# Kernel tuning notes

Measured on AMD Instinct MI355X. Metric: run time of the kernel, lower is better.

## Reference

```python
import jax, jax.numpy as jnp
import numpy as np

B, S, E, H = 1, 2048, 1024, 16
D = E // H  # head_dim = 64


def setup_inputs() -> dict:
    key = jax.random.key(0)
    ks = jax.random.split(key, 9)
    sd = 0.02
    hidden_states = jax.random.normal(ks[0], (B, S, E), dtype=jnp.float32)
    # causal mask: positions with mask==0 are filled with -inf (per masked_fill_)
    mask = jnp.tril(jnp.ones((1, 1, S, S), dtype=bool))
    Wq = jax.random.normal(ks[1], (E, E), dtype=jnp.float32) * sd
    bq = jax.random.normal(ks[2], (E,), dtype=jnp.float32) * sd
    Wk = jax.random.normal(ks[3], (D, E), dtype=jnp.float32) * sd
    bk = jax.random.normal(ks[4], (D,), dtype=jnp.float32) * sd
    Wv = jax.random.normal(ks[5], (D, E), dtype=jnp.float32) * sd
    bv = jax.random.normal(ks[6], (D,), dtype=jnp.float32) * sd
    Wo = jax.random.normal(ks[7], (E, E), dtype=jnp.float32) * sd
    bo = jax.random.normal(ks[8], (E,), dtype=jnp.float32) * sd
    return {"hidden_states": hidden_states, "mask": mask,
            "Wq": Wq, "bq": bq, "Wk": Wk, "bk": bk,
            "Wv": Wv, "bv": bv, "Wo": Wo, "bo": bo}


def reference(hidden_states, mask, Wq, bq, Wk, bk, Wv, bv, Wo, bo):
    bsz, tgt_len, embed_dim = hidden_states.shape
    # projections (torch Linear: x @ W^T + b)
    q = hidden_states @ Wq.T + bq                       # [B, S, E]
    q = q.reshape(bsz, tgt_len, H, D).transpose(0, 2, 1, 3)  # [B, H, S, D]
    k = hidden_states @ Wk.T + bk                       # [B, S, D] shared single KV head
    v = hidden_states @ Wv.T + bv                       # [B, S, D]
    scaling = jnp.sqrt(jnp.asarray(D, dtype=hidden_states.dtype))
    # QK^T with implicit broadcast of the shared K head (instead of expand)
    scores = jnp.einsum('bhqd,bkd->bhqk', q, k) / scaling   # [B, H, S, S]
    scores = jnp.where(mask, scores, -jnp.inf)
    probs = jax.nn.softmax(scores, axis=-1)             # dropout p=0 -> identity
    attn = jnp.einsum('bhqk,bkd->bhqd', probs, v)       # [B, H, S, D]
    attn = attn.transpose(0, 2, 1, 3).reshape(bsz, tgt_len, H * D)
    return attn @ Wo.T + bo                             # [B, S, E]
```

## Files before the change

kernel.cpp:

```cpp
#include <hip/hip_runtime.h>
#include <hip/hip_bf16.h>

typedef __hip_bfloat16 bf16;
typedef __attribute__((ext_vector_type(8))) short short8;
typedef __attribute__((ext_vector_type(4))) float f32x4;

__device__ __forceinline__ short8 ld8(const void* p) { return *(const short8*)p; }
__device__ __forceinline__ void st8(void* p, short8 v) { *(short8*)p = v; }

__device__ __forceinline__ void async_cp16(bf16* lds, const bf16* g) {
    __builtin_amdgcn_global_load_lds(
        (const __attribute__((address_space(1))) unsigned int*)g,
        (__attribute__((address_space(3))) unsigned int*)lds, 16, 0, 0);
}

struct bf4 { bf16 a, b, c, d; };

__global__ void cast_kernel(const float* __restrict__ s0, bf16* __restrict__ d0, int n0_,
                            const float* __restrict__ s1, bf16* __restrict__ d1, int n1_,
                            const float* __restrict__ s2, bf16* __restrict__ d2, int n2_,
                            const float* __restrict__ s3, bf16* __restrict__ d3, int n3_,
                            const float* __restrict__ s4, bf16* __restrict__ d4, int n4_) {
    const float* srcs[5] = {s0, s1, s2, s3, s4};
    bf16* dsts[5] = {d0, d1, d2, d3, d4};
    int ns[5] = {n0_, n1_, n2_, n3_, n4_};
    int stride = gridDim.x * blockDim.x;
    int t0 = blockIdx.x * blockDim.x + threadIdx.x;
#pragma unroll
    for (int a = 0; a < 5; ++a) {
        const float4* src = (const float4*)srcs[a];
        bf4* dst = (bf4*)dsts[a];
        int n4 = ns[a] >> 2;
        for (int i = t0; i < n4; i += stride) {
            float4 v = src[i];
            bf4 o = {__float2bfloat16(v.x), __float2bfloat16(v.y),
                     __float2bfloat16(v.z), __float2bfloat16(v.w)};
            dst[i] = o;
        }
    }
}

__global__ void qkv_proj_kernel(const bf16* __restrict__ A,
                                const bf16* __restrict__ Wq, const bf16* __restrict__ Wk,
                                const bf16* __restrict__ Wv,
                                const float* __restrict__ bq, const float* __restrict__ bk,
                                const float* __restrict__ bv,
                                bf16* __restrict__ qo, bf16* __restrict__ ko,
                                bf16* __restrict__ vto, int M, int K) {
    __shared__ __align__(16) bf16 As[128][64];
    __shared__ __align__(16) bf16 Bs[64][64];
    const int nt = blockIdx.x;
    const bf16* W;
    const float* bias;
    int mode, nw0;
    if (nt < 16)      { W = Wq; bias = bq; mode = 0; nw0 = nt * 64; }
    else if (nt == 16){ W = Wk; bias = bk; mode = 1; nw0 = 0; }
    else              { W = Wv; bias = bv; mode = 2; nw0 = 0; }

    const int tid = threadIdx.x;
    const int wave = tid >> 6, lane = tid & 63;
    const int l16 = lane & 15, quad = lane >> 4;
    const int m0 = blockIdx.y * 128;
    const int lr = lane >> 3, lsw = (lane & 7) ^ (lr & 7);

    f32x4 acc[2][4];
    const f32x4 z = {0.f, 0.f, 0.f, 0.f};
#pragma unroll
    for (int mi = 0; mi < 2; ++mi)
#pragma unroll
        for (int ni = 0; ni < 4; ++ni) acc[mi][ni] = z;

    for (int k0 = 0; k0 < K; k0 += 64) {
#pragma unroll
        for (int u = 0; u < 4; ++u) {
            int t = wave * 4 + u;
            async_cp16(&As[t * 8][0], A + (size_t)(m0 + t * 8 + lr) * K + k0 + lsw * 8);
        }
#pragma unroll
        for (int u = 0; u < 2; ++u) {
            int t = wave * 2 + u;
            async_cp16(&Bs[t * 8][0], W + (size_t)(nw0 + t * 8 + lr) * K + k0 + lsw * 8);
        }
        __syncthreads();

        short8 af[2][2], bfr[2][4];
#pragma unroll
        for (int mi = 0; mi < 2; ++mi)
#pragma unroll
            for (int kc = 0; kc < 2; ++kc) {
                int R = wave * 32 + mi * 16 + l16;
                int g = kc * 4 + quad;
                af[mi][kc] = ld8(&As[R][(g ^ (R & 7)) * 8]);
            }
#pragma unroll
        for (int ni = 0; ni < 4; ++ni)
#pragma unroll
            for (int kc = 0; kc < 2; ++kc) {
                int r = ni * 16 + l16;
                int g = kc * 4 + quad;
                bfr[kc][ni] = ld8(&Bs[r][(g ^ (r & 7)) * 8]);
            }
#pragma unroll
        for (int kc = 0; kc < 2; ++kc)
#pragma unroll
            for (int mi = 0; mi < 2; ++mi)
#pragma unroll
                for (int ni = 0; ni < 4; ++ni)
                    acc[mi][ni] = __builtin_amdgcn_mfma_f32_16x16x32_bf16(
                        af[mi][kc], bfr[kc][ni], acc[mi][ni], 0, 0, 0);
        __syncthreads();
    }

#pragma unroll
    for (int mi = 0; mi < 2; ++mi)
#pragma unroll
        for (int ni = 0; ni < 4; ++ni)
#pragma unroll
            for (int r = 0; r < 4; ++r) {
                int row = m0 + wave * 32 + mi * 16 + quad * 4 + r;
                int col = ni * 16 + l16;
                float v = acc[mi][ni][r] + bias[nw0 + col];
                if (mode == 0)
                    qo[(size_t)row * 1024 + nt * 64 + col] = __float2bfloat16(v * 0.125f);
                else if (mode == 1)
                    ko[(size_t)row * 64 + col] = __float2bfloat16(v);
                else
                    vto[(size_t)col * M + row] = __float2bfloat16(v);
            }
}

__global__ void gemm_bt_mfma(const bf16* __restrict__ A, const bf16* __restrict__ W,
                             const float* __restrict__ bias, float* __restrict__ C,
                             int M, int N, int K) {
    __shared__ __align__(16) bf16 As[128][64];
    __shared__ __align__(16) bf16 Bs[64][64];
    const int tid = threadIdx.x;
    const int wave = tid >> 6, lane = tid & 63;
    const int l16 = lane & 15, quad = lane >> 4;
    const int m0 = blockIdx.y * 128, n0 = blockIdx.x * 64;
    const int lr = lane >> 3, lsw = (lane & 7) ^ (lr & 7);

    f32x4 acc[2][4];
    const f32x4 z = {0.f, 0.f, 0.f, 0.f};
#pragma unroll
    for (int mi = 0; mi < 2; ++mi)
#pragma unroll
        for (int ni = 0; ni < 4; ++ni) acc[mi][ni] = z;

    for (int k0 = 0; k0 < K; k0 += 64) {
#pragma unroll
        for (int u = 0; u < 4; ++u) {
            int t = wave * 4 + u;
            async_cp16(&As[t * 8][0], A + (size_t)(m0 + t * 8 + lr) * K + k0 + lsw * 8);
        }
#pragma unroll
        for (int u = 0; u < 2; ++u) {
            int t = wave * 2 + u;
            async_cp16(&Bs[t * 8][0], W + (size_t)(n0 + t * 8 + lr) * K + k0 + lsw * 8);
        }
        __syncthreads();

        short8 af[2][2], bfr[2][4];
#pragma unroll
        for (int mi = 0; mi < 2; ++mi)
#pragma unroll
            for (int kc = 0; kc < 2; ++kc) {
                int R = wave * 32 + mi * 16 + l16;
                int g = kc * 4 + quad;
                af[mi][kc] = ld8(&As[R][(g ^ (R & 7)) * 8]);
            }
#pragma unroll
        for (int ni = 0; ni < 4; ++ni)
#pragma unroll
            for (int kc = 0; kc < 2; ++kc) {
                int r = ni * 16 + l16;
                int g = kc * 4 + quad;
                bfr[kc][ni] = ld8(&Bs[r][(g ^ (r & 7)) * 8]);
            }
#pragma unroll
        for (int kc = 0; kc < 2; ++kc)
#pragma unroll
            for (int mi = 0; mi < 2; ++mi)
#pragma unroll
                for (int ni = 0; ni < 4; ++ni)
                    acc[mi][ni] = __builtin_amdgcn_mfma_f32_16x16x32_bf16(
                        af[mi][kc], bfr[kc][ni], acc[mi][ni], 0, 0, 0);
        __syncthreads();
    }

#pragma unroll
    for (int mi = 0; mi < 2; ++mi)
#pragma unroll
        for (int ni = 0; ni < 4; ++ni)
#pragma unroll
            for (int r = 0; r < 4; ++r) {
                int row = m0 + wave * 32 + mi * 16 + quad * 4 + r;
                int col = n0 + ni * 16 + l16;
                C[(size_t)row * N + col] = acc[mi][ni][r] + bias[col];
            }
}

__global__ void flash_mfma_kernel(const bf16* __restrict__ Q, const bf16* __restrict__ Kg,
                                  const bf16* __restrict__ VT,
                                  float* __restrict__ Opart, float* __restrict__ Lpart,
                                  int S) {
    const int s = blockIdx.x;
    int i, c;
    if (s < 32)      { c = 0; i = s; }
    else if (s < 56) { c = 1; i = s - 24; }
    else if (s < 72) { c = 2; i = s - 40; }
    else             { c = 3; i = s - 48; }

    __shared__ __align__(16) bf16 Ks[2][64][64];
    __shared__ __align__(16) bf16 Vt[2][64][64];
    __shared__ bf16 Ps[4][16][68];

    const int h = blockIdx.y;
    const int q0 = i * 64;
    const int tid = threadIdx.x;
    const int wave = tid >> 6, lane = tid & 63;
    const int l16 = lane & 15, quad = lane >> 4;
    const int lr = lane >> 3, lsw = (lane & 7) ^ (lr & 7);
    const int qrow = q0 + wave * 16;

    short8 qf[2];
#pragma unroll
    for (int kc = 0; kc < 2; ++kc)
        qf[kc] = ld8(Q + (size_t)(qrow + l16) * 1024 + h * 64 + kc * 32 + quad * 8);

    short8 onesf;
    {
        short o = (l16 == 0) ? (short)0x3F80 : (short)0;
        onesf[0]=o; onesf[1]=o; onesf[2]=o; onesf[3]=o;
        onesf[4]=o; onesf[5]=o; onesf[6]=o; onesf[7]=o;
    }

    f32x4 of[4];
    const f32x4 z = {0.f, 0.f, 0.f, 0.f};
#pragma unroll
    for (int dt = 0; dt < 4; ++dt) of[dt] = z;
    f32x4 lacc = z;

    const int jt0 = c * 8;
    const int jt1 = min(c * 8 + 8, i + 1);

    {
        const int j0 = jt0 * 64;
#pragma unroll
        for (int u = 0; u < 2; ++u) {
            int t = wave * 2 + u;
            async_cp16(&Ks[0][t * 8][0], Kg + (size_t)(j0 + t * 8 + lr) * 64 + lsw * 8);
            async_cp16(&Vt[0][t * 8][0], VT + (size_t)(t * 8 + lr) * S + j0 + lsw * 8);
        }
    }

    int buf = 0;
    for (int jt = jt0; jt < jt1; ++jt, buf ^= 1) {
        __syncthreads();
        if (jt + 1 < jt1) {
            const int j0n = (jt + 1) * 64;
#pragma unroll
            for (int u = 0; u < 2; ++u) {
                int t = wave * 2 + u;
                async_cp16(&Ks[buf ^ 1][t * 8][0], Kg + (size_t)(j0n + t * 8 + lr) * 64 + lsw * 8);
                async_cp16(&Vt[buf ^ 1][t * 8][0], VT + (size_t)(t * 8 + lr) * S + j0n + lsw * 8);
            }
        }
        const int j0 = jt * 64;

        f32x4 sc[4];
#pragma unroll
        for (int nt = 0; nt < 4; ++nt) {
            int R = nt * 16 + l16;
            sc[nt] = __builtin_amdgcn_mfma_f32_16x16x32_bf16(
                qf[0], ld8(&Ks[buf][R][(quad ^ (R & 7)) * 8]), z, 0, 0, 0);
            sc[nt] = __builtin_amdgcn_mfma_f32_16x16x32_bf16(
                qf[1], ld8(&Ks[buf][R][((4 + quad) ^ (R & 7)) * 8]), sc[nt], 0, 0, 0);
        }
        bool need_mask = (j0 + 63 > qrow);
        if (need_mask) {
#pragma unroll
            for (int nt = 0; nt < 4; ++nt)
#pragma unroll
                for (int r = 0; r < 4; ++r)
                    if (j0 + nt * 16 + l16 > qrow + quad * 4 + r) sc[nt][r] = -1e30f;
        }

#pragma unroll
        for (int nt = 0; nt < 4; ++nt)
#pragma unroll
            for (int r = 0; r < 4; ++r)
                Ps[wave][quad * 4 + r][nt * 16 + l16] = __float2bfloat16(__expf(sc[nt][r]));

        short8 pf[2];
        pf[0] = ld8(&Ps[wave][l16][quad * 8]);
        pf[1] = ld8(&Ps[wave][l16][32 + quad * 8]);

        lacc = __builtin_amdgcn_mfma_f32_16x16x32_bf16(pf[0], onesf, lacc, 0, 0, 0);
        lacc = __builtin_amdgcn_mfma_f32_16x16x32_bf16(pf[1], onesf, lacc, 0, 0, 0);

#pragma unroll
        for (int dt = 0; dt < 4; ++dt) {
            int R = dt * 16 + l16;
            of[dt] = __builtin_amdgcn_mfma_f32_16x16x32_bf16(
                pf[0], ld8(&Vt[buf][R][(quad ^ (R & 7)) * 8]), of[dt], 0, 0, 0);
            of[dt] = __builtin_amdgcn_mfma_f32_16x16x32_bf16(
                pf[1], ld8(&Vt[buf][R][((4 + quad) ^ (R & 7)) * 8]), of[dt], 0, 0, 0);
        }
    }

    float* Op = Opart + ((size_t)s * 16 + h) * 4096;
#pragma unroll
    for (int dt = 0; dt < 4; ++dt)
#pragma unroll
        for (int r = 0; r < 4; ++r) {
            int row = wave * 16 + quad * 4 + r;
            Op[row * 64 + dt * 16 + l16] = of[dt][r];
        }
    if (l16 == 0) {
        float* L = Lpart + ((size_t)s * 16 + h) * 64;
#pragma unroll
        for (int r = 0; r < 4; ++r)
            L[wave * 16 + quad * 4 + r] = lacc[r];
    }
}

__global__ void flash_merge_kernel(const float* __restrict__ Opart,
                                   const float* __restrict__ Lpart,
                                   bf16* __restrict__ attn) {
    const int i = blockIdx.x, h = blockIdx.y;
    const int nch = (i >> 3) + 1;
    const int tid = threadIdx.x;
    const int row = tid >> 2, cg = (tid & 3) * 16;

    float L = 0.f;
    for (int cc = 0; cc < nch; ++cc) {
        int s = (cc == 0) ? i : (cc == 1) ? 24 + i : (cc == 2) ? 40 + i : 48 + i;
        L += Lpart[((size_t)s * 16 + h) * 64 + row];
    }
    float inv = 1.f / L;

    float o[16];
#pragma unroll
    for (int j = 0; j < 16; ++j) o[j] = 0.f;
    for (int cc = 0; cc < nch; ++cc) {
        int s = (cc == 0) ? i : (cc == 1) ? 24 + i : (cc == 2) ? 40 + i : 48 + i;
        const float* Op = Opart + ((size_t)s * 16 + h) * 4096 + row * 64 + cg;
#pragma unroll
        for (int j = 0; j < 16; ++j) o[j] += Op[j];
    }
    bf16* dst = attn + (size_t)(i * 64 + row) * 1024 + h * 64 + cg;
#pragma unroll
    for (int j = 0; j < 16; ++j) dst[j] = __float2bfloat16(o[j] * inv);
}

extern "C" void kernel_launch(void* const* d_in, const int* in_sizes, int n_in,
                              void* d_out, int out_size, void* d_ws, size_t ws_size,
                              hipStream_t stream) {
    const int S = 2048, E = 1024, D = 64;

    const float* hs = (const float*)d_in[0];
    const float* Wq = (const float*)d_in[2];
    const float* bq = (const float*)d_in[3];
    const float* Wk = (const float*)d_in[4];
    const float* bk = (const float*)d_in[5];
    const float* Wv = (const float*)d_in[6];
    const float* bv = (const float*)d_in[7];
    const float* Wo = (const float*)d_in[8];
    const float* bo = (const float*)d_in[9];
    float* out = (float*)d_out;

    bf16* ws = (bf16*)d_ws;
    bf16* hsb = ws;
    bf16* wqb = hsb + (size_t)S * E;
    bf16* wkb = wqb + (size_t)E * E;
    bf16* wvb = wkb + (size_t)D * E;
    bf16* wob = wvb + (size_t)D * E;
    bf16* q = wob + (size_t)E * E;
    bf16* kbuf = q + (size_t)S * E;
    bf16* vt = kbuf + (size_t)S * D;
    bf16* attn = vt + (size_t)S * D;
    float* Opart = (float*)(attn + (size_t)S * E);
    float* Lpart = Opart + (size_t)1280 * 4096;

    dim3 blk(256);
    cast_kernel<<<512, blk, 0, stream>>>(hs, hsb, S * E,
                                         Wq, wqb, E * E,
                                         Wk, wkb, D * E,
                                         Wv, wvb, D * E,
                                         Wo, wob, E * E);
    qkv_proj_kernel<<<dim3(18, S / 128), blk, 0, stream>>>(hsb, wqb, wkb, wvb,
                                                           bq, bk, bv,
                                                           q, kbuf, vt, S, E);
    flash_mfma_kernel<<<dim3(80, 16), blk, 0, stream>>>(q, kbuf, vt, Opart, Lpart, S);
    flash_merge_kernel<<<dim3(32, 16), blk, 0, stream>>>(Opart, Lpart, attn);
    gemm_bt_mfma<<<dim3(E / 64, S / 128), blk, 0, stream>>>(attn, wob, bo, out, S, E, E);
}
```

Before: 160.6 us.

## Retile GEMMs to 64x64 with K=128 stages, halve flash splits, store partials in bf16

```diff
diff --git a/kernel.cpp b/kernel.cpp
--- a/kernel.cpp
+++ b/kernel.cpp
@@ -6,7 +6,6 @@
 typedef __attribute__((ext_vector_type(4))) float f32x4;
 
 __device__ __forceinline__ short8 ld8(const void* p) { return *(const short8*)p; }
-__device__ __forceinline__ void st8(void* p, short8 v) { *(short8*)p = v; }
 
 __device__ __forceinline__ void async_cp16(bf16* lds, const bf16* g) {
     __builtin_amdgcn_global_load_lds(
@@ -40,6 +39,15 @@
     }
 }
 
+#define GEMM_STAGE(dst, src_base, row0, ldk)                                   \
+    _Pragma("unroll")                                                          \
+    for (int u = 0; u < 4; ++u) {                                              \
+        int t = wave * 4 + u;                                                  \
+        int row = t * 4 + (lane >> 4);                                         \
+        int gsrc = (lane & 15) ^ (row & 15);                                   \
+        async_cp16(&dst[t * 4][0], src_base + (size_t)(row0 + row) * ldk + k0 + gsrc * 8); \
+    }
+
 __global__ void qkv_proj_kernel(const bf16* __restrict__ A,
                                 const bf16* __restrict__ Wq, const bf16* __restrict__ Wk,
                                 const bf16* __restrict__ Wv,
@@ -47,8 +55,8 @@
                                 const float* __restrict__ bv,
                                 bf16* __restrict__ qo, bf16* __restrict__ ko,
                                 bf16* __restrict__ vto, int M, int K) {
-    __shared__ __align__(16) bf16 As[128][64];
-    __shared__ __align__(16) bf16 Bs[64][64];
+    __shared__ __align__(16) bf16 As[64][128];
+    __shared__ __align__(16) bf16 Bs[64][128];
     const int nt = blockIdx.x;
     const bf16* W;
     const float* bias;
@@ -60,156 +68,117 @@
     const int tid = threadIdx.x;
     const int wave = tid >> 6, lane = tid & 63;
     const int l16 = lane & 15, quad = lane >> 4;
-    const int m0 = blockIdx.y * 128;
-    const int lr = lane >> 3, lsw = (lane & 7) ^ (lr & 7);
-
-    f32x4 acc[2][4];
+    const int m0 = blockIdx.y * 64;
+
+    f32x4 acc[4];
     const f32x4 z = {0.f, 0.f, 0.f, 0.f};
 #pragma unroll
-    for (int mi = 0; mi < 2; ++mi)
-#pragma unroll
-        for (int ni = 0; ni < 4; ++ni) acc[mi][ni] = z;
-
-    for (int k0 = 0; k0 < K; k0 += 64) {
-#pragma unroll
-        for (int u = 0; u < 4; ++u) {
-            int t = wave * 4 + u;
-            async_cp16(&As[t * 8][0], A + (size_t)(m0 + t * 8 + lr) * K + k0 + lsw * 8);
-        }
-#pragma unroll
-        for (int u = 0; u < 2; ++u) {
-            int t = wave * 2 + u;
-            async_cp16(&Bs[t * 8][0], W + (size_t)(nw0 + t * 8 + lr) * K + k0 + lsw * 8);
-        }
-        __syncthreads();
-
-        short8 af[2][2], bfr[2][4];
-#pragma unroll
-        for (int mi = 0; mi < 2; ++mi)
-#pragma unroll
-            for (int kc = 0; kc < 2; ++kc) {
-                int R = wave * 32 + mi * 16 + l16;
-                int g = kc * 4 + quad;
-                af[mi][kc] = ld8(&As[R][(g ^ (R & 7)) * 8]);
-            }
-#pragma unroll
-        for (int ni = 0; ni < 4; ++ni)
-#pragma unroll
-            for (int kc = 0; kc < 2; ++kc) {
-                int r = ni * 16 + l16;
-                int g = kc * 4 + quad;
-                bfr[kc][ni] = ld8(&Bs[r][(g ^ (r & 7)) * 8]);
-            }
-#pragma unroll
-        for (int kc = 0; kc < 2; ++kc)
-#pragma unroll
-            for (int mi = 0; mi < 2; ++mi)
-#pragma unroll
-                for (int ni = 0; ni < 4; ++ni)
-                    acc[mi][ni] = __builtin_amdgcn_mfma_f32_16x16x32_bf16(
-                        af[mi][kc], bfr[kc][ni], acc[mi][ni], 0, 0, 0);
-        __syncthreads();
-    }
-
-#pragma unroll
-    for (int mi = 0; mi < 2; ++mi)
-#pragma unroll
-        for (int ni = 0; ni < 4; ++ni)
-#pragma unroll
-            for (int r = 0; r < 4; ++r) {
-                int row = m0 + wave * 32 + mi * 16 + quad * 4 + r;
-                int col = ni * 16 + l16;
-                float v = acc[mi][ni][r] + bias[nw0 + col];
-                if (mode == 0)
-                    qo[(size_t)row * 1024 + nt * 64 + col] = __float2bfloat16(v * 0.125f);
-                else if (mode == 1)
-                    ko[(size_t)row * 64 + col] = __float2bfloat16(v);
-                else
-                    vto[(size_t)col * M + row] = __float2bfloat16(v);
-            }
+    for (int ni = 0; ni < 4; ++ni) acc[ni] = z;
+
+    for (int k0 = 0; k0 < K; k0 += 128) {
+        GEMM_STAGE(As, A, m0, K)
+        GEMM_STAGE(Bs, W, nw0, K)
+        __syncthreads();
+
+        short8 af[4], bfr[4][4];
+        {
+            int R = wave * 16 + l16;
+#pragma unroll
+            for (int kc = 0; kc < 4; ++kc)
+                af[kc] = ld8(&As[R][((kc * 4 + quad) ^ (R & 15)) * 8]);
+        }
+#pragma unroll
+        for (int ni = 0; ni < 4; ++ni) {
+            int r = ni * 16 + l16;
+#pragma unroll
+            for (int kc = 0; kc < 4; ++kc)
+                bfr[kc][ni] = ld8(&Bs[r][((kc * 4 + quad) ^ (r & 15)) * 8]);
+        }
+#pragma unroll
+        for (int kc = 0; kc < 4; ++kc)
+#pragma unroll
+            for (int ni = 0; ni < 4; ++ni)
+                acc[ni] = __builtin_amdgcn_mfma_f32_16x16x32_bf16(
+                    af[kc], bfr[kc][ni], acc[ni], 0, 0, 0);
+        __syncthreads();
+    }
+
+#pragma unroll
+    for (int ni = 0; ni < 4; ++ni)
+#pragma unroll
+        for (int r = 0; r < 4; ++r) {
+            int row = m0 + wave * 16 + quad * 4 + r;
+            int col = ni * 16 + l16;
+            float v = acc[ni][r] + bias[nw0 + col];
+            if (mode == 0)
+                qo[(size_t)row * 1024 + nt * 64 + col] = __float2bfloat16(v * 0.125f);
+            else if (mode == 1)
+                ko[(size_t)row * 64 + col] = __float2bfloat16(v);
+            else
+                vto[(size_t)col * M + row] = __float2bfloat16(v);
+        }
 }
 
 __global__ void gemm_bt_mfma(const bf16* __restrict__ A, const bf16* __restrict__ W,
                              const float* __restrict__ bias, float* __restrict__ C,
                              int M, int N, int K) {
-    __shared__ __align__(16) bf16 As[128][64];
-    __shared__ __align__(16) bf16 Bs[64][64];
+    __shared__ __align__(16) bf16 As[64][128];
+    __shared__ __align__(16) bf16 Bs[64][128];
     const int tid = threadIdx.x;
     const int wave = tid >> 6, lane = tid & 63;
     const int l16 = lane & 15, quad = lane >> 4;
-    const int m0 = blockIdx.y * 128, n0 = blockIdx.x * 64;
-    const int lr = lane >> 3, lsw = (lane & 7) ^ (lr & 7);
-
-    f32x4 acc[2][4];
+    const int m0 = blockIdx.y * 64, n0 = blockIdx.x * 64;
+
+    f32x4 acc[4];
     const f32x4 z = {0.f, 0.f, 0.f, 0.f};
 #pragma unroll
-    for (int mi = 0; mi < 2; ++mi)
-#pragma unroll
-        for (int ni = 0; ni < 4; ++ni) acc[mi][ni] = z;
-
-    for (int k0 = 0; k0 < K; k0 += 64) {
-#pragma unroll
-        for (int u = 0; u < 4; ++u) {
-            int t = wave * 4 + u;
-            async_cp16(&As[t * 8][0], A + (size_t)(m0 + t * 8 + lr) * K + k0 + lsw * 8);
-        }
-#pragma unroll
-        for (int u = 0; u < 2; ++u) {
-            int t = wave * 2 + u;
-            async_cp16(&Bs[t * 8][0], W + (size_t)(n0 + t * 8 + lr) * K + k0 + lsw * 8);
-        }
-        __syncthreads();
-
-        short8 af[2][2], bfr[2][4];
-#pragma unroll
-        for (int mi = 0; mi < 2; ++mi)
-#pragma unroll
-            for (int kc = 0; kc < 2; ++kc) {
-                int R = wave * 32 + mi * 16 + l16;
-                int g = kc * 4 + quad;
-                af[mi][kc] = ld8(&As[R][(g ^ (R & 7)) * 8]);
-            }
-#pragma unroll
-        for (int ni = 0; ni < 4; ++ni)
-#pragma unroll
-            for (int kc = 0; kc < 2; ++kc) {
-                int r = ni * 16 + l16;
-                int g = kc * 4 + quad;
-                bfr[kc][ni] = ld8(&Bs[r][(g ^ (r & 7)) * 8]);
-            }
-#pragma unroll
-        for (int kc = 0; kc < 2; ++kc)
-#pragma unroll
-            for (int mi = 0; mi < 2; ++mi)
-#pragma unroll
-                for (int ni = 0; ni < 4; ++ni)
-                    acc[mi][ni] = __builtin_amdgcn_mfma_f32_16x16x32_bf16(
-                        af[mi][kc], bfr[kc][ni], acc[mi][ni], 0, 0, 0);
-        __syncthreads();
-    }
-
-#pragma unroll
-    for (int mi = 0; mi < 2; ++mi)
-#pragma unroll
-        for (int ni = 0; ni < 4; ++ni)
-#pragma unroll
-            for (int r = 0; r < 4; ++r) {
-                int row = m0 + wave * 32 + mi * 16 + quad * 4 + r;
-                int col = n0 + ni * 16 + l16;
-                C[(size_t)row * N + col] = acc[mi][ni][r] + bias[col];
-            }
+    for (int ni = 0; ni < 4; ++ni) acc[ni] = z;
+
+    for (int k0 = 0; k0 < K; k0 += 128) {
+        GEMM_STAGE(As, A, m0, K)
+        GEMM_STAGE(Bs, W, n0, K)
+        __syncthreads();
+
+        short8 af[4], bfr[4][4];
+        {
+            int R = wave * 16 + l16;
+#pragma unroll
+            for (int kc = 0; kc < 4; ++kc)
+                af[kc] = ld8(&As[R][((kc * 4 + quad) ^ (R & 15)) * 8]);
+        }
+#pragma unroll
+        for (int ni = 0; ni < 4; ++ni) {
+            int r = ni * 16 + l16;
+#pragma unroll
+            for (int kc = 0; kc < 4; ++kc)
+                bfr[kc][ni] = ld8(&Bs[r][((kc * 4 + quad) ^ (r & 15)) * 8]);
+        }
+#pragma unroll
+        for (int kc = 0; kc < 4; ++kc)
+#pragma unroll
+            for (int ni = 0; ni < 4; ++ni)
+                acc[ni] = __builtin_amdgcn_mfma_f32_16x16x32_bf16(
+                    af[kc], bfr[kc][ni], acc[ni], 0, 0, 0);
+        __syncthreads();
+    }
+
+#pragma unroll
+    for (int ni = 0; ni < 4; ++ni)
+#pragma unroll
+        for (int r = 0; r < 4; ++r) {
+            int row = m0 + wave * 16 + quad * 4 + r;
+            int col = n0 + ni * 16 + l16;
+            C[(size_t)row * N + col] = acc[ni][r] + bias[col];
+        }
 }
 
 __global__ void flash_mfma_kernel(const bf16* __restrict__ Q, const bf16* __restrict__ Kg,
                                   const bf16* __restrict__ VT,
-                                  float* __restrict__ Opart, float* __restrict__ Lpart,
+                                  bf16* __restrict__ Opart, float* __restrict__ Lpart,
                                   int S) {
     const int s = blockIdx.x;
-    int i, c;
-    if (s < 32)      { c = 0; i = s; }
-    else if (s < 56) { c = 1; i = s - 24; }
-    else if (s < 72) { c = 2; i = s - 40; }
-    else             { c = 3; i = s - 48; }
+    const int c = (s >= 32) ? 1 : 0;
+    const int i = (c == 0) ? s : s - 16;
 
     __shared__ __align__(16) bf16 Ks[2][64][64];
     __shared__ __align__(16) bf16 Vt[2][64][64];
@@ -241,8 +210,8 @@
     for (int dt = 0; dt < 4; ++dt) of[dt] = z;
     f32x4 lacc = z;
 
-    const int jt0 = c * 8;
-    const int jt1 = min(c * 8 + 8, i + 1);
+    const int jt0 = c * 16;
+    const int jt1 = min(c * 16 + 16, i + 1);
 
     {
         const int j0 = jt0 * 64;
@@ -309,13 +278,13 @@
         }
     }
 
-    float* Op = Opart + ((size_t)s * 16 + h) * 4096;
+    bf16* Op = Opart + ((size_t)s * 16 + h) * 4096;
 #pragma unroll
     for (int dt = 0; dt < 4; ++dt)
 #pragma unroll
         for (int r = 0; r < 4; ++r) {
             int row = wave * 16 + quad * 4 + r;
-            Op[row * 64 + dt * 16 + l16] = of[dt][r];
+            Op[row * 64 + dt * 16 + l16] = __float2bfloat16(of[dt][r]);
         }
     if (l16 == 0) {
         float* L = Lpart + ((size_t)s * 16 + h) * 64;
@@ -325,17 +294,17 @@
     }
 }
 
-__global__ void flash_merge_kernel(const float* __restrict__ Opart,
+__global__ void flash_merge_kernel(const bf16* __restrict__ Opart,
                                    const float* __restrict__ Lpart,
                                    bf16* __restrict__ attn) {
     const int i = blockIdx.x, h = blockIdx.y;
-    const int nch = (i >> 3) + 1;
+    const int nch = (i >> 4) + 1;
     const int tid = threadIdx.x;
     const int row = tid >> 2, cg = (tid & 3) * 16;
 
     float L = 0.f;
     for (int cc = 0; cc < nch; ++cc) {
-        int s = (cc == 0) ? i : (cc == 1) ? 24 + i : (cc == 2) ? 40 + i : 48 + i;
+        int s = (cc == 0) ? i : 16 + i;
         L += Lpart[((size_t)s * 16 + h) * 64 + row];
     }
     float inv = 1.f / L;
@@ -344,10 +313,10 @@
 #pragma unroll
     for (int j = 0; j < 16; ++j) o[j] = 0.f;
     for (int cc = 0; cc < nch; ++cc) {
-        int s = (cc == 0) ? i : (cc == 1) ? 24 + i : (cc == 2) ? 40 + i : 48 + i;
-        const float* Op = Opart + ((size_t)s * 16 + h) * 4096 + row * 64 + cg;
-#pragma unroll
-        for (int j = 0; j < 16; ++j) o[j] += Op[j];
+        int s = (cc == 0) ? i : 16 + i;
+        const bf16* Op = Opart + ((size_t)s * 16 + h) * 4096 + row * 64 + cg;
+#pragma unroll
+        for (int j = 0; j < 16; ++j) o[j] += __bfloat162float(Op[j]);
     }
     bf16* dst = attn + (size_t)(i * 64 + row) * 1024 + h * 64 + cg;
 #pragma unroll
@@ -380,8 +349,8 @@
     bf16* kbuf = q + (size_t)S * E;
     bf16* vt = kbuf + (size_t)S * D;
     bf16* attn = vt + (size_t)S * D;
-    float* Opart = (float*)(attn + (size_t)S * E);
-    float* Lpart = Opart + (size_t)1280 * 4096;
+    bf16* Opart = attn + (size_t)S * E;
+    float* Lpart = (float*)(Opart + (size_t)768 * 4096);
 
     dim3 blk(256);
     cast_kernel<<<512, blk, 0, stream>>>(hs, hsb, S * E,
@@ -389,10 +358,10 @@
                                          Wk, wkb, D * E,
                                          Wv, wvb, D * E,
                                          Wo, wob, E * E);
-    qkv_proj_kernel<<<dim3(18, S / 128), blk, 0, stream>>>(hsb, wqb, wkb, wvb,
-                                                           bq, bk, bv,
-                                                           q, kbuf, vt, S, E);
-    flash_mfma_kernel<<<dim3(80, 16), blk, 0, stream>>>(q, kbuf, vt, Opart, Lpart, S);
+    qkv_proj_kernel<<<dim3(18, S / 64), blk, 0, stream>>>(hsb, wqb, wkb, wvb,
+                                                          bq, bk, bv,
+                                                          q, kbuf, vt, S, E);
+    flash_mfma_kernel<<<dim3(48, 16), blk, 0, stream>>>(q, kbuf, vt, Opart, Lpart, S);
     flash_merge_kernel<<<dim3(32, 16), blk, 0, stream>>>(Opart, Lpart, attn);
-    gemm_bt_mfma<<<dim3(E / 64, S / 128), blk, 0, stream>>>(attn, wob, bo, out, S, E, E);
-}
+    gemm_bt_mfma<<<dim3(E / 64, S / 64), blk, 0, stream>>>(attn, wob, bo, out, S, E, E);
+}
```

New measurement: 152.2 us. 1.06x faster.
